# Kernel tuning notes

Hardware: AMD Instinct MI355X
Metric: run time of the kernel (lower is better)

## Reference

```python
import jax, jax.numpy as jnp
import numpy as np

HEADS = 4


def setup_inputs() -> dict:
    key = jax.random.key(0)
    ks = jax.random.split(key, 6)
    b, c, d, h, w = 4, 512, 16, 16, 16
    x = jax.random.normal(ks[0], (b, c, d, h, w), dtype=jnp.float32)
    s = 0.02  # param init scale
    Wq = jax.random.normal(ks[1], (c, c), dtype=jnp.float32) * s
    Wk = jax.random.normal(ks[2], (c, c), dtype=jnp.float32) * s
    Wv = jax.random.normal(ks[3], (c, c), dtype=jnp.float32) * s
    Wproj = jax.random.normal(ks[4], (c, c), dtype=jnp.float32) * s
    bproj = jnp.zeros((c,), dtype=jnp.float32)
    return {"x": x, "Wq": Wq, "Wk": Wk, "Wv": Wv, "Wproj": Wproj, "bproj": bproj}


def reference(x, Wq, Wk, Wv, Wproj, bproj):
    b, c, d, h, w = x.shape
    N = d * h * w
    scale = (c // HEADS) ** -0.5  # module uses ch//heads for scale
    xf = x.reshape(b, c, N)  # (b, c, N)
    # 1x1 Conv1d == channel matmul
    q = jnp.einsum('oc,bcn->bon', Wq, xf)
    k = jnp.einsum('oc,bcn->bon', Wk, xf)
    v = jnp.einsum('oc,bcn->bon', Wv, xf)
    # Faithful to original (buggy) view: split SEQUENCE dim by heads -> (b, H, c, N//H)
    q = q.reshape(b, HEADS, c, N // HEADS)
    k = k.reshape(b, HEADS, c, N // HEADS)
    v = v.reshape(b, HEADS, c, N // HEADS)
    attn = jax.nn.softmax(jnp.einsum('bhqe,bhke->bhqk', q, k) * scale, axis=-1)
    out = jnp.einsum('bhqk,bhke->bhqe', attn, v)  # (b, H, c, N//H)
    out = jnp.swapaxes(out, 2, 3).reshape(b, c, N)  # matches transpose(2,3).view
    out = jnp.einsum('oc,bcn->bon', Wproj, out) + bproj[None, :, None]
    return out.reshape(b, c, d, h, w) + x
```

## Files before the change

kernel.cpp:

```cpp
#include <hip/hip_runtime.h>
#include <stdint.h>


typedef __attribute__((ext_vector_type(8))) short short8;
typedef __attribute__((ext_vector_type(4))) float f32x4;

typedef const __attribute__((address_space(1))) unsigned int* gas_ptr;
typedef __attribute__((address_space(3))) unsigned int* las_ptr;

#define ATTN_SCALE 0.08838834764831845f

__device__ __forceinline__ unsigned short f2bf(float f) {
    union { float f; unsigned int u; } c; c.f = f;
    unsigned int u = c.u;
    u += 0x7fffu + ((u >> 16) & 1u);
    return (unsigned short)(u >> 16);
}

__device__ __forceinline__ void gl_lds16(const void* g, void* l) {
    __builtin_amdgcn_global_load_lds((gas_ptr)(uintptr_t)g, (las_ptr)(uintptr_t)l,
                                     16, 0, 0);
}

template<int LDA, int LDB, int KDIM, bool PERMB = false>
__device__ __forceinline__ void mfma_core(
    const unsigned short* __restrict__ A,
    const unsigned short* __restrict__ B,
    int m0, int n0,
    unsigned short* __restrict__ sA, unsigned short* __restrict__ sB,
    f32x4 acc[4][4])
{
    const int tid  = threadIdx.x;
    const int lane = tid & 63, wave = tid >> 6;
    const int lr = lane >> 2, lc = lane & 3;
    const int wm = (wave & 1) * 64, wn = (wave >> 1) * 64;
    const int col = lane & 15, quad = lane >> 4;

    const unsigned short* ga = A + (size_t)(m0 + 32 * wave + lr) * LDA + lc * 8;
    int rb0 = n0 + 32 * wave + lr;
    int rb1 = rb0 + 16;
    if (PERMB) {
        rb0 = 4 * (rb0 & 127) + (rb0 >> 7);
        rb1 = 4 * (rb1 & 127) + (rb1 >> 7);
    }
    const unsigned short* gb0 = B + (size_t)rb0 * LDB + lc * 8;
    const unsigned short* gb1 = B + (size_t)rb1 * LDB + lc * 8;

    unsigned short* la0 = sA + (32 * wave) * 32;
    unsigned short* la1 = sA + (32 * wave + 16) * 32;
    unsigned short* lb0 = sB + (32 * wave) * 32;
    unsigned short* lb1 = sB + (32 * wave + 16) * 32;

    for (int k0 = 0; k0 < KDIM; k0 += 32) {
        gl_lds16(ga + k0,            la0);
        gl_lds16(ga + k0 + 16 * LDA, la1);
        gl_lds16(gb0 + k0,           lb0);
        gl_lds16(gb1 + k0,           lb1);
        __syncthreads();
        short8 af[4], bf[4];
        #pragma unroll
        for (int i = 0; i < 4; ++i)
            af[i] = *(const short8*)&sA[(wm + i * 16 + col) * 32 + quad * 8];
        #pragma unroll
        for (int j = 0; j < 4; ++j)
            bf[j] = *(const short8*)&sB[(wn + j * 16 + col) * 32 + quad * 8];
        #pragma unroll
        for (int i = 0; i < 4; ++i)
            #pragma unroll
            for (int j = 0; j < 4; ++j)
                acc[i][j] = __builtin_amdgcn_mfma_f32_16x16x32_bf16(
                    af[i], bf[j], acc[i][j], 0, 0, 0);
        __syncthreads();
    }
}

__global__ __launch_bounds__(256)
void prep(const float* __restrict__ x,
          const float* __restrict__ Wq, const float* __restrict__ Wk,
          const float* __restrict__ Wv, const float* __restrict__ Wp,
          unsigned short* __restrict__ xT, unsigned short* __restrict__ Wb)
{
    if (blockIdx.z == 4) {
        const int idx = (blockIdx.y * 64 + blockIdx.x) * 256 + threadIdx.x;
        const int mat = idx >> 16;
        const int off = (idx & 65535) << 2;
        const float* src = (mat == 0 ? Wq : mat == 1 ? Wk : mat == 2 ? Wv : Wp) + off;
        const float4 f = *(const float4*)src;
        uint2 o;
        o.x = f2bf(f.x) | ((unsigned)f2bf(f.y) << 16);
        o.y = f2bf(f.z) | ((unsigned)f2bf(f.w) << 16);
        *(uint2*)&Wb[mat * 262144 + off] = o;
        return;
    }
    const int b = blockIdx.z;
    const int l = threadIdx.x & 63, w = threadIdx.x >> 6;
    const int n  = blockIdx.x * 64 + l;
    const int c0 = blockIdx.y * 32 + w * 8;
    const float* xp = x + (size_t)b * 2097152 + (size_t)c0 * 4096 + n;
    unsigned int p[4];
    #pragma unroll
    for (int j = 0; j < 4; ++j) {
        const unsigned short a  = f2bf(xp[(2 * j)     * 4096]);
        const unsigned short bb = f2bf(xp[(2 * j + 1) * 4096]);
        p[j] = a | ((unsigned)bb << 16);
    }
    uint4 v; v.x = p[0]; v.y = p[1]; v.z = p[2]; v.w = p[3];
    *(uint4*)&xT[(size_t)b * 2097152 + (size_t)n * 512 + c0] = v;
}

__global__ __launch_bounds__(256)
void gemm_qkv(const unsigned short* __restrict__ Wb,
              const unsigned short* __restrict__ xT,
              unsigned short* __restrict__ qb, unsigned short* __restrict__ kb,
              unsigned short* __restrict__ vT)
{
    __shared__ unsigned short sA[128 * 32], sB[128 * 32];

    const int z = blockIdx.z, wsel = z >> 2, b = z & 3;
    const unsigned short* A = Wb + wsel * 262144;
    const unsigned short* B = xT + (size_t)b * 2097152;
    const int m0 = blockIdx.y * 128, n0 = blockIdx.x * 128;

    f32x4 z4 = {0.f, 0.f, 0.f, 0.f};
    f32x4 acc[4][4];
    #pragma unroll
    for (int i = 0; i < 4; ++i)
        #pragma unroll
        for (int j = 0; j < 4; ++j) acc[i][j] = z4;

    mfma_core<512, 512, 512>(A, B, m0, n0, sA, sB, acc);

    const int lane = threadIdx.x & 63, wave = threadIdx.x >> 6;
    const int wm = (wave & 1) * 64, wn = (wave >> 1) * 64;
    const int col = lane & 15, quad = lane >> 4;

    if (wsel < 2) {
        unsigned short* C = (wsel == 0 ? qb : kb) + (size_t)b * 2097152;
        #pragma unroll
        for (int i = 0; i < 4; ++i)
            #pragma unroll
            for (int r = 0; r < 4; ++r) {
                const int row = m0 + wm + i * 16 + quad * 4 + r;
                #pragma unroll
                for (int j = 0; j < 4; ++j)
                    C[(size_t)row * 4096 + n0 + wn + j * 16 + col] = f2bf(acc[i][j][r]);
            }
    } else {
        const int h = m0 >> 7, s = n0 >> 10, e0 = n0 & 1023;
        unsigned short* dst = vT + (size_t)(b * 4 + h) * 524288 + s * 128;
        #pragma unroll
        for (int i = 0; i < 4; ++i) {
            const int kb2 = wm + i * 16 + quad * 4;
            #pragma unroll
            for (int j = 0; j < 4; ++j) {
                const int e = e0 + wn + j * 16 + col;
                uint2 o;
                o.x = f2bf(acc[i][j][0]) | ((unsigned)f2bf(acc[i][j][1]) << 16);
                o.y = f2bf(acc[i][j][2]) | ((unsigned)f2bf(acc[i][j][3]) << 16);
                *(uint2*)&dst[(size_t)e * 512 + kb2] = o;
            }
        }
    }
}

__global__ __launch_bounds__(256)
void gemm_qk(const unsigned short* __restrict__ qb,
             const unsigned short* __restrict__ kb,
             float* __restrict__ S)
{
    __shared__ unsigned short sA[128 * 32], sB[128 * 32];
    const int z = blockIdx.z;
    const int slab = z >> 1, half = z & 1;
    const unsigned short* A = qb + (size_t)slab * 524288 + half * 512;
    const unsigned short* B = kb + (size_t)slab * 524288 + half * 512;
    float* Sp = S + (size_t)half * 4194304 + (size_t)slab * 262144;
    const int m0 = blockIdx.y * 128, n0 = blockIdx.x * 128;

    f32x4 z4 = {0.f, 0.f, 0.f, 0.f};
    f32x4 acc[4][4];
    #pragma unroll
    for (int i = 0; i < 4; ++i)
        #pragma unroll
        for (int j = 0; j < 4; ++j) acc[i][j] = z4;

    mfma_core<1024, 1024, 512, true>(A, B, m0, n0, sA, sB, acc);

    const int lane = threadIdx.x & 63, wave = threadIdx.x >> 6;
    const int wm = (wave & 1) * 64, wn = (wave >> 1) * 64;
    const int col = lane & 15, quad = lane >> 4;
    #pragma unroll
    for (int i = 0; i < 4; ++i)
        #pragma unroll
        for (int r = 0; r < 4; ++r) {
            const int row = m0 + wm + i * 16 + quad * 4 + r;
            #pragma unroll
            for (int j = 0; j < 4; ++j)
                Sp[(size_t)row * 512 + n0 + wn + j * 16 + col] =
                    acc[i][j][r] * ATTN_SCALE;
        }
}

__global__ __launch_bounds__(256)
void softmax_rows(const float* __restrict__ S, unsigned short* __restrict__ P)
{
    const int wave = threadIdx.x >> 6, lane = threadIdx.x & 63;
    const int row  = blockIdx.x * 4 + wave;
    const float* p0 = S + (size_t)row * 512;
    const float* p1 = p0 + 4194304;
    unsigned short* o = P + (size_t)row * 512;

    float vals[8];
    float m = -1e30f;
    #pragma unroll
    for (int t = 0; t < 8; ++t) {
        vals[t] = p0[lane + t * 64] + p1[lane + t * 64];
        m = fmaxf(m, vals[t]);
    }
    #pragma unroll
    for (int s = 32; s > 0; s >>= 1) m = fmaxf(m, __shfl_xor(m, s));
    float sum = 0.f;
    #pragma unroll
    for (int t = 0; t < 8; ++t) { vals[t] = __expf(vals[t] - m); sum += vals[t]; }
    #pragma unroll
    for (int s = 32; s > 0; s >>= 1) sum += __shfl_xor(sum, s);
    const float inv = 1.f / sum;
    #pragma unroll
    for (int t = 0; t < 8; ++t) o[lane + t * 64] = f2bf(vals[t] * inv);
}

__global__ __launch_bounds__(256)
void gemm_pv(const unsigned short* __restrict__ Pb,
             const unsigned short* __restrict__ vT,
             unsigned short* __restrict__ yT)
{
    __shared__ unsigned short sT[128 * 136];
    unsigned short* sA = sT;
    unsigned short* sB = sT + 4096;
    const int z = blockIdx.z, b = z >> 2, hh = z & 3;
    const unsigned short* A = Pb + (size_t)z * 262144;
    const unsigned short* B = vT + (size_t)z * 524288;
    unsigned short* yTb = yT + (size_t)b * 2097152;
    const int m0 = blockIdx.y * 128;
    const int n0 = blockIdx.x * 128;

    f32x4 z4 = {0.f, 0.f, 0.f, 0.f};
    f32x4 acc[4][4];
    #pragma unroll
    for (int i = 0; i < 4; ++i)
        #pragma unroll
        for (int j = 0; j < 4; ++j) acc[i][j] = z4;

    mfma_core<512, 512, 512>(A, B, m0, n0, sA, sB, acc);

    const int tid = threadIdx.x;
    const int lane = tid & 63, wave = tid >> 6;
    const int wm = (wave & 1) * 64, wn = (wave >> 1) * 64;
    const int col = lane & 15, quad = lane >> 4;

    #pragma unroll
    for (int i = 0; i < 4; ++i)
        #pragma unroll
        for (int r = 0; r < 4; ++r) {
            const int rr = wm + i * 16 + quad * 4 + r;
            #pragma unroll
            for (int j = 0; j < 4; ++j)
                sT[rr * 136 + wn + j * 16 + col] = f2bf(acc[i][j][r]);
        }
    __syncthreads();

    #pragma unroll
    for (int k = 0; k < 4; ++k) {
        const int rid = k * 256 + tid;
        const int qq_l = rid >> 3, s = rid & 7;
        const unsigned short* Trow = sT + qq_l * 136;
        unsigned int p[8];
        #pragma unroll
        for (int t = 0; t < 8; ++t) {
            const unsigned int a  = Trow[s + 8 * (2 * t)];
            const unsigned int bb = Trow[s + 8 * (2 * t + 1)];
            p[t] = a | (bb << 16);
        }
        const size_t base = (size_t)((s << 9) + m0 + qq_l) * 512 + hh * 128 + (n0 >> 3);
        uint4 lo; lo.x = p[0]; lo.y = p[1]; lo.z = p[2]; lo.w = p[3];
        uint4 hi; hi.x = p[4]; hi.y = p[5]; hi.z = p[6]; hi.w = p[7];
        *(uint4*)&yTb[base]     = lo;
        *(uint4*)&yTb[base + 8] = hi;
    }
}

__global__ __launch_bounds__(256)
void gemm_proj(const unsigned short* __restrict__ Wpb,
               const unsigned short* __restrict__ yT,
               const float* __restrict__ bias, const float* __restrict__ x,
               float* __restrict__ out)
{
    __shared__ unsigned short sA[128 * 32], sB[128 * 32];
    const int b = blockIdx.z;
    const unsigned short* B = yT + (size_t)b * 2097152;
    const int m0 = blockIdx.y * 128, n0 = blockIdx.x * 128;

    f32x4 z4 = {0.f, 0.f, 0.f, 0.f};
    f32x4 acc[4][4];
    #pragma unroll
    for (int i = 0; i < 4; ++i)
        #pragma unroll
        for (int j = 0; j < 4; ++j) acc[i][j] = z4;

    mfma_core<512, 512, 512>(Wpb, B, m0, n0, sA, sB, acc);

    const int lane = threadIdx.x & 63, wave = threadIdx.x >> 6;
    const int wm = (wave & 1) * 64, wn = (wave >> 1) * 64;
    const int col = lane & 15, quad = lane >> 4;
    const size_t boff = (size_t)b * 2097152;
    #pragma unroll
    for (int i = 0; i < 4; ++i)
        #pragma unroll
        for (int r = 0; r < 4; ++r) {
            const int row = m0 + wm + i * 16 + quad * 4 + r;
            const float bi = bias[row];
            #pragma unroll
            for (int j = 0; j < 4; ++j) {
                const size_t idx = boff + (size_t)row * 4096 + n0 + wn + j * 16 + col;
                out[idx] = acc[i][j][r] + bi + x[idx];
            }
        }
}

extern "C" void kernel_launch(void* const* d_in, const int* in_sizes, int n_in,
                              void* d_out, int out_size, void* d_ws, size_t ws_size,
                              hipStream_t stream) {
    const float* x     = (const float*)d_in[0];
    const float* Wq    = (const float*)d_in[1];
    const float* Wk    = (const float*)d_in[2];
    const float* Wv    = (const float*)d_in[3];
    const float* Wproj = (const float*)d_in[4];
    const float* bproj = (const float*)d_in[5];
    float* out = (float*)d_out;

    char* w = (char*)d_ws;
    unsigned short* xT = (unsigned short*)(w + 0);
    unsigned short* qb = (unsigned short*)(w + 16777216);
    unsigned short* kb = (unsigned short*)(w + 33554432);
    unsigned short* vT = (unsigned short*)(w + 50331648);
    float*          S  = (float*)        (w + 67108864);
    unsigned short* Pb = (unsigned short*)(w + 100663296);
    unsigned short* Wb = (unsigned short*)(w + 109051904);
    unsigned short* yT = xT;

    prep        <<<dim3(64, 16, 5),  256, 0, stream>>>(x, Wq, Wk, Wv, Wproj, xT, Wb);
    gemm_qkv    <<<dim3(32, 4, 12),  256, 0, stream>>>(Wb, xT, qb, kb, vT);
    gemm_qk     <<<dim3(4, 4, 32),   256, 0, stream>>>(qb, kb, S);
    softmax_rows<<<dim3(2048),       256, 0, stream>>>(S, Pb);
    gemm_pv     <<<dim3(8, 4, 16),   256, 0, stream>>>(Pb, vT, yT);
    gemm_proj   <<<dim3(32, 4, 4),   256, 0, stream>>>(Wb + 3 * 262144, yT, bproj, x, out);
}
```

Before: 206.1 us.

## Fuse QK^T scores and row softmax into one kernel, dropping fp32 score buffer

Result: slower. 211.3 us (+2.5%).

```diff
diff --git a/kernel.cpp b/kernel.cpp
--- a/kernel.cpp
+++ b/kernel.cpp
@@ -163,69 +163,160 @@
     }
 }
 
-__global__ __launch_bounds__(256)
-void gemm_qk(const unsigned short* __restrict__ qb,
-             const unsigned short* __restrict__ kb,
-             float* __restrict__ S)
-{
-    __shared__ unsigned short sA[128 * 32], sB[128 * 32];
-    const int z = blockIdx.z;
-    const int slab = z >> 1, half = z & 1;
-    const unsigned short* A = qb + (size_t)slab * 524288 + half * 512;
-    const unsigned short* B = kb + (size_t)slab * 524288 + half * 512;
-    float* Sp = S + (size_t)half * 4194304 + (size_t)slab * 262144;
-    const int m0 = blockIdx.y * 128, n0 = blockIdx.x * 128;
+__global__ __launch_bounds__(512)
+void qk_softmax(const unsigned short* __restrict__ qb,
+                const unsigned short* __restrict__ kb,
+                unsigned short* __restrict__ Pb)
+{
+    __shared__ unsigned short sQ[32 * 32];
+    __shared__ unsigned short sK[512 * 32];
+    __shared__ float sStat[8][32];
+
+    const int tid = threadIdx.x;
+    const int lane = tid & 63, wave = tid >> 6;
+    const int col = lane & 15, quad = lane >> 4;
+    const int lr = lane >> 2, lc = lane & 3;
+    const int slab = blockIdx.y;
+    const int m0 = blockIdx.x * 32;
+    const int cbase = wave * 64;
+
+    const unsigned short* Q = qb + (size_t)slab * 524288;
+    const unsigned short* K = kb + (size_t)slab * 524288;
+
+    const unsigned short* gq = (wave < 2)
+        ? Q + (size_t)(m0 + wave * 16 + lr) * 1024 + lc * 8 : nullptr;
+    const unsigned short* gk[4];
+    #pragma unroll
+    for (int t = 0; t < 4; ++t) {
+        const int kkp = (wave * 4 + t) * 16 + lr;
+        const int phys = 4 * (kkp & 127) + (kkp >> 7);
+        gk[t] = K + (size_t)phys * 1024 + lc * 8;
+    }
 
     f32x4 z4 = {0.f, 0.f, 0.f, 0.f};
-    f32x4 acc[4][4];
-    #pragma unroll
-    for (int i = 0; i < 4; ++i)
+    f32x4 acc[2][4];
+    #pragma unroll
+    for (int i = 0; i < 2; ++i)
         #pragma unroll
         for (int j = 0; j < 4; ++j) acc[i][j] = z4;
 
-    mfma_core<1024, 1024, 512, true>(A, B, m0, n0, sA, sB, acc);
-
-    const int lane = threadIdx.x & 63, wave = threadIdx.x >> 6;
-    const int wm = (wave & 1) * 64, wn = (wave >> 1) * 64;
-    const int col = lane & 15, quad = lane >> 4;
-    #pragma unroll
-    for (int i = 0; i < 4; ++i)
-        #pragma unroll
-        for (int r = 0; r < 4; ++r) {
-            const int row = m0 + wm + i * 16 + quad * 4 + r;
+    for (int k0 = 0; k0 < 1024; k0 += 32) {
+        #pragma unroll
+        for (int t = 0; t < 4; ++t)
+            gl_lds16(gk[t] + k0, sK + (wave * 4 + t) * 512);
+        if (wave < 2)
+            gl_lds16(gq + k0, sQ + wave * 512);
+        __syncthreads();
+        short8 af[2], bf[4];
+        #pragma unroll
+        for (int i = 0; i < 2; ++i)
+            af[i] = *(const short8*)&sQ[(i * 16 + col) * 32 + quad * 8];
+        #pragma unroll
+        for (int j = 0; j < 4; ++j)
+            bf[j] = *(const short8*)&sK[(cbase + j * 16 + col) * 32 + quad * 8];
+        #pragma unroll
+        for (int i = 0; i < 2; ++i)
             #pragma unroll
             for (int j = 0; j < 4; ++j)
-                Sp[(size_t)row * 512 + n0 + wn + j * 16 + col] =
-                    acc[i][j][r] * ATTN_SCALE;
-        }
-}
-
-__global__ __launch_bounds__(256)
-void softmax_rows(const float* __restrict__ S, unsigned short* __restrict__ P)
-{
-    const int wave = threadIdx.x >> 6, lane = threadIdx.x & 63;
-    const int row  = blockIdx.x * 4 + wave;
-    const float* p0 = S + (size_t)row * 512;
-    const float* p1 = p0 + 4194304;
-    unsigned short* o = P + (size_t)row * 512;
-
-    float vals[8];
-    float m = -1e30f;
-    #pragma unroll
-    for (int t = 0; t < 8; ++t) {
-        vals[t] = p0[lane + t * 64] + p1[lane + t * 64];
-        m = fmaxf(m, vals[t]);
-    }
-    #pragma unroll
-    for (int s = 32; s > 0; s >>= 1) m = fmaxf(m, __shfl_xor(m, s));
-    float sum = 0.f;
-    #pragma unroll
-    for (int t = 0; t < 8; ++t) { vals[t] = __expf(vals[t] - m); sum += vals[t]; }
-    #pragma unroll
-    for (int s = 32; s > 0; s >>= 1) sum += __shfl_xor(sum, s);
-    const float inv = 1.f / sum;
-    #pragma unroll
-    for (int t = 0; t < 8; ++t) o[lane + t * 64] = f2bf(vals[t] * inv);
+                acc[i][j] = __builtin_amdgcn_mfma_f32_16x16x32_bf16(
+                    af[i], bf[j], acc[i][j], 0, 0, 0);
+        __syncthreads();
+    }
+
+    float mx[2][4];
+    #pragma unroll
+    for (int i = 0; i < 2; ++i)
+        #pragma unroll
+        for (int r = 0; r < 4; ++r) {
+            float m = acc[i][0][r];
+            #pragma unroll
+            for (int j = 1; j < 4; ++j) m = fmaxf(m, acc[i][j][r]);
+            mx[i][r] = m;
+        }
+    #pragma unroll
+    for (int s = 1; s < 16; s <<= 1)
+        #pragma unroll
+        for (int i = 0; i < 2; ++i)
+            #pragma unroll
+            for (int r = 0; r < 4; ++r)
+                mx[i][r] = fmaxf(mx[i][r], __shfl_xor(mx[i][r], s));
+    if (col == 0)
+        #pragma unroll
+        for (int i = 0; i < 2; ++i)
+            #pragma unroll
+            for (int r = 0; r < 4; ++r)
+                sStat[wave][i * 16 + quad * 4 + r] = mx[i][r];
+    __syncthreads();
+    float M[2][4];
+    #pragma unroll
+    for (int i = 0; i < 2; ++i)
+        #pragma unroll
+        for (int r = 0; r < 4; ++r) {
+            const int row = i * 16 + quad * 4 + r;
+            float m = sStat[0][row];
+            #pragma unroll
+            for (int w = 1; w < 8; ++w) m = fmaxf(m, sStat[w][row]);
+            M[i][r] = m;
+        }
+    __syncthreads();
+
+    float sm[2][4] = {};
+    #pragma unroll
+    for (int i = 0; i < 2; ++i)
+        #pragma unroll
+        for (int r = 0; r < 4; ++r) {
+            #pragma unroll
+            for (int j = 0; j < 4; ++j) {
+                const float e = __expf((acc[i][j][r] - M[i][r]) * ATTN_SCALE);
+                acc[i][j][r] = e;
+                sm[i][r] += e;
+            }
+        }
+    #pragma unroll
+    for (int s = 1; s < 16; s <<= 1)
+        #pragma unroll
+        for (int i = 0; i < 2; ++i)
+            #pragma unroll
+            for (int r = 0; r < 4; ++r)
+                sm[i][r] += __shfl_xor(sm[i][r], s);
+    if (col == 0)
+        #pragma unroll
+        for (int i = 0; i < 2; ++i)
+            #pragma unroll
+            for (int r = 0; r < 4; ++r)
+                sStat[wave][i * 16 + quad * 4 + r] = sm[i][r];
+    __syncthreads();
+    float inv[2][4];
+    #pragma unroll
+    for (int i = 0; i < 2; ++i)
+        #pragma unroll
+        for (int r = 0; r < 4; ++r) {
+            const int row = i * 16 + quad * 4 + r;
+            float s = sStat[0][row];
+            #pragma unroll
+            for (int w = 1; w < 8; ++w) s += sStat[w][row];
+            inv[i][r] = 1.f / s;
+        }
+
+    unsigned short* sP = sK;
+    #pragma unroll
+    for (int i = 0; i < 2; ++i)
+        #pragma unroll
+        for (int r = 0; r < 4; ++r) {
+            const int row = i * 16 + quad * 4 + r;
+            #pragma unroll
+            for (int j = 0; j < 4; ++j)
+                sP[row * 512 + cbase + j * 16 + col] = f2bf(acc[i][j][r] * inv[i][r]);
+        }
+    __syncthreads();
+
+    unsigned short* dst = Pb + (size_t)slab * 262144 + (size_t)m0 * 512;
+    #pragma unroll
+    for (int u = 0; u < 4; ++u) {
+        const int c = u * 512 + tid;
+        const int row = c >> 6, ch = c & 63;
+        *(uint4*)&dst[(size_t)row * 512 + ch * 8] = *(const uint4*)&sP[row * 512 + ch * 8];
+    }
 }
 
 __global__ __launch_bounds__(256)
@@ -342,15 +433,13 @@
     unsigned short* qb = (unsigned short*)(w + 16777216);
     unsigned short* kb = (unsigned short*)(w + 33554432);
     unsigned short* vT = (unsigned short*)(w + 50331648);
-    float*          S  = (float*)        (w + 67108864);
-    unsigned short* Pb = (unsigned short*)(w + 100663296);
-    unsigned short* Wb = (unsigned short*)(w + 109051904);
+    unsigned short* Pb = (unsigned short*)(w + 67108864);
+    unsigned short* Wb = (unsigned short*)(w + 75497472);
     unsigned short* yT = xT;
 
-    prep        <<<dim3(64, 16, 5),  256, 0, stream>>>(x, Wq, Wk, Wv, Wproj, xT, Wb);
-    gemm_qkv    <<<dim3(32, 4, 12),  256, 0, stream>>>(Wb, xT, qb, kb, vT);
-    gemm_qk     <<<dim3(4, 4, 32),   256, 0, stream>>>(qb, kb, S);
-    softmax_rows<<<dim3(2048),       256, 0, stream>>>(S, Pb);
-    gemm_pv     <<<dim3(8, 4, 16),   256, 0, stream>>>(Pb, vT, yT);
-    gemm_proj   <<<dim3(32, 4, 4),   256, 0, stream>>>(Wb + 3 * 262144, yT, bproj, x, out);
-}
+    prep       <<<dim3(64, 16, 5),  256, 0, stream>>>(x, Wq, Wk, Wv, Wproj, xT, Wb);
+    gemm_qkv   <<<dim3(32, 4, 12),  256, 0, stream>>>(Wb, xT, qb, kb, vT);
+    qk_softmax <<<dim3(16, 16),     512, 0, stream>>>(qb, kb, Pb);
+    gemm_pv    <<<dim3(8, 4, 16),   256, 0, stream>>>(Pb, vT, yT);
+    gemm_proj  <<<dim3(32, 4, 4),   256, 0, stream>>>(Wb + 3 * 262144, yT, bproj, x, out);
+}
```

## Fuse softmax into PV GEMM with deferred row normalisation

Applied to the files above, without the earlier changes.

New measurement: 223.7 us. +8.5%, slower.

```diff
diff --git a/kernel.cpp b/kernel.cpp
--- a/kernel.cpp
+++ b/kernel.cpp
@@ -201,48 +201,40 @@
 }
 
 __global__ __launch_bounds__(256)
-void softmax_rows(const float* __restrict__ S, unsigned short* __restrict__ P)
-{
-    const int wave = threadIdx.x >> 6, lane = threadIdx.x & 63;
-    const int row  = blockIdx.x * 4 + wave;
-    const float* p0 = S + (size_t)row * 512;
-    const float* p1 = p0 + 4194304;
-    unsigned short* o = P + (size_t)row * 512;
-
-    float vals[8];
-    float m = -1e30f;
-    #pragma unroll
-    for (int t = 0; t < 8; ++t) {
-        vals[t] = p0[lane + t * 64] + p1[lane + t * 64];
-        m = fmaxf(m, vals[t]);
-    }
-    #pragma unroll
-    for (int s = 32; s > 0; s >>= 1) m = fmaxf(m, __shfl_xor(m, s));
-    float sum = 0.f;
-    #pragma unroll
-    for (int t = 0; t < 8; ++t) { vals[t] = __expf(vals[t] - m); sum += vals[t]; }
-    #pragma unroll
-    for (int s = 32; s > 0; s >>= 1) sum += __shfl_xor(sum, s);
-    const float inv = 1.f / sum;
-    #pragma unroll
-    for (int t = 0; t < 8; ++t) o[lane + t * 64] = f2bf(vals[t] * inv);
-}
-
-__global__ __launch_bounds__(256)
-void gemm_pv(const unsigned short* __restrict__ Pb,
-             const unsigned short* __restrict__ vT,
-             unsigned short* __restrict__ yT)
+void gemm_pv_sm(const float* __restrict__ S,
+                const unsigned short* __restrict__ vT,
+                unsigned short* __restrict__ yT)
 {
     __shared__ unsigned short sT[128 * 136];
+    __shared__ float sLh[256];
     unsigned short* sA = sT;
     unsigned short* sB = sT + 4096;
+
     const int z = blockIdx.z, b = z >> 2, hh = z & 3;
-    const unsigned short* A = Pb + (size_t)z * 262144;
+    const float* S0 = S + (size_t)z * 262144;
+    const float* S1 = S0 + 4194304;
     const unsigned short* B = vT + (size_t)z * 524288;
     unsigned short* yTb = yT + (size_t)b * 2097152;
     const int m0 = blockIdx.y * 128;
     const int n0 = blockIdx.x * 128;
 
+    const int tid = threadIdx.x;
+    const int lane = tid & 63, wave = tid >> 6;
+    const int lr = lane >> 2, lc = lane & 3;
+    const int wm = (wave & 1) * 64, wn = (wave >> 1) * 64;
+    const int col = lane & 15, quad = lane >> 4;
+
+    const unsigned short* gb0 = B + (size_t)(n0 + 32 * wave + lr) * 512 + lc * 8;
+    const unsigned short* gb1 = gb0 + (size_t)16 * 512;
+    unsigned short* lb0 = sB + (32 * wave) * 32;
+    unsigned short* lb1 = sB + (32 * wave + 16) * 32;
+
+    const int srow = tid >> 1;
+    const int shalf = (tid & 1) << 4;
+    const float* s0p = S0 + (size_t)(m0 + srow) * 512 + shalf;
+    const float* s1p = S1 + (size_t)(m0 + srow) * 512 + shalf;
+    unsigned short* sArow = sA + srow * 32 + shalf;
+
     f32x4 z4 = {0.f, 0.f, 0.f, 0.f};
     f32x4 acc[4][4];
     #pragma unroll
@@ -250,12 +242,59 @@
         #pragma unroll
         for (int j = 0; j < 4; ++j) acc[i][j] = z4;
 
-    mfma_core<512, 512, 512>(A, B, m0, n0, sA, sB, acc);
-
-    const int tid = threadIdx.x;
-    const int lane = tid & 63, wave = tid >> 6;
-    const int wm = (wave & 1) * 64, wn = (wave >> 1) * 64;
-    const int col = lane & 15, quad = lane >> 4;
+    float lpart = 0.f;
+
+    for (int k0 = 0; k0 < 512; k0 += 32) {
+        gl_lds16(gb0 + k0, lb0);
+        gl_lds16(gb1 + k0, lb1);
+        float v[16];
+        #pragma unroll
+        for (int t = 0; t < 4; ++t) {
+            const float4 a0 = *(const float4*)&s0p[k0 + t * 4];
+            const float4 a1 = *(const float4*)&s1p[k0 + t * 4];
+            v[t * 4 + 0] = a0.x + a1.x; v[t * 4 + 1] = a0.y + a1.y;
+            v[t * 4 + 2] = a0.z + a1.z; v[t * 4 + 3] = a0.w + a1.w;
+        }
+        unsigned int pk[8];
+        #pragma unroll
+        for (int t = 0; t < 8; ++t) {
+            const float e0 = __expf(fminf(v[2 * t],     80.f));
+            const float e1 = __expf(fminf(v[2 * t + 1], 80.f));
+            lpart += e0 + e1;
+            pk[t] = f2bf(e0) | ((unsigned)f2bf(e1) << 16);
+        }
+        uint4 lo; lo.x = pk[0]; lo.y = pk[1]; lo.z = pk[2]; lo.w = pk[3];
+        uint4 hi; hi.x = pk[4]; hi.y = pk[5]; hi.z = pk[6]; hi.w = pk[7];
+        *(uint4*)&sArow[0] = lo;
+        *(uint4*)&sArow[8] = hi;
+        __syncthreads();
+        short8 af[4], bf[4];
+        #pragma unroll
+        for (int i = 0; i < 4; ++i)
+            af[i] = *(const short8*)&sA[(wm + i * 16 + col) * 32 + quad * 8];
+        #pragma unroll
+        for (int j = 0; j < 4; ++j)
+            bf[j] = *(const short8*)&sB[(wn + j * 16 + col) * 32 + quad * 8];
+        #pragma unroll
+        for (int i = 0; i < 4; ++i)
+            #pragma unroll
+            for (int j = 0; j < 4; ++j)
+                acc[i][j] = __builtin_amdgcn_mfma_f32_16x16x32_bf16(
+                    af[i], bf[j], acc[i][j], 0, 0, 0);
+        __syncthreads();
+    }
+
+    sLh[tid] = lpart;
+    __syncthreads();
+
+    float inv[4][4];
+    #pragma unroll
+    for (int i = 0; i < 4; ++i)
+        #pragma unroll
+        for (int r = 0; r < 4; ++r) {
+            const int row = wm + i * 16 + quad * 4 + r;
+            inv[i][r] = 1.f / (sLh[2 * row] + sLh[2 * row + 1]);
+        }
 
     #pragma unroll
     for (int i = 0; i < 4; ++i)
@@ -264,7 +303,7 @@
             const int rr = wm + i * 16 + quad * 4 + r;
             #pragma unroll
             for (int j = 0; j < 4; ++j)
-                sT[rr * 136 + wn + j * 16 + col] = f2bf(acc[i][j][r]);
+                sT[rr * 136 + wn + j * 16 + col] = f2bf(acc[i][j][r] * inv[i][r]);
         }
     __syncthreads();
 
@@ -343,14 +382,12 @@
     unsigned short* kb = (unsigned short*)(w + 33554432);
     unsigned short* vT = (unsigned short*)(w + 50331648);
     float*          S  = (float*)        (w + 67108864);
-    unsigned short* Pb = (unsigned short*)(w + 100663296);
-    unsigned short* Wb = (unsigned short*)(w + 109051904);
+    unsigned short* Wb = (unsigned short*)(w + 100663296);
     unsigned short* yT = xT;
 
-    prep        <<<dim3(64, 16, 5),  256, 0, stream>>>(x, Wq, Wk, Wv, Wproj, xT, Wb);
-    gemm_qkv    <<<dim3(32, 4, 12),  256, 0, stream>>>(Wb, xT, qb, kb, vT);
-    gemm_qk     <<<dim3(4, 4, 32),   256, 0, stream>>>(qb, kb, S);
-    softmax_rows<<<dim3(2048),       256, 0, stream>>>(S, Pb);
-    gemm_pv     <<<dim3(8, 4, 16),   256, 0, stream>>>(Pb, vT, yT);
-    gemm_proj   <<<dim3(32, 4, 4),   256, 0, stream>>>(Wb + 3 * 262144, yT, bproj, x, out);
-}
+    prep       <<<dim3(64, 16, 5),  256, 0, stream>>>(x, Wq, Wk, Wv, Wproj, xT, Wb);
+    gemm_qkv   <<<dim3(32, 4, 12),  256, 0, stream>>>(Wb, xT, qb, kb, vT);
+    gemm_qk    <<<dim3(4, 4, 32),   256, 0, stream>>>(qb, kb, S);
+    gemm_pv_sm <<<dim3(8, 4, 16),   256, 0, stream>>>(S, vT, yT);
+    gemm_proj  <<<dim3(32, 4, 4),   256, 0, stream>>>(Wb + 3 * 262144, yT, bproj, x, out);
+}
```
